# Performance work log

Hardware: AMD Instinct MI355X
Metric: run time of the kernel (lower is better)

The kernel has to match this reference:

```python
import jax, jax.numpy as jnp
import numpy as np

N = 768
C = 1024            # box_head representation size
HID = 256           # RePN hidden / gcn_hidden
HEADS1 = 4
K = 5               # topk neighbors
NEG_SLOPE = 0.2


def setup_inputs() -> dict:
    key = jax.random.key(0)
    ks = jax.random.split(key, 24)
    feats = jax.random.normal(ks[0], (N, C), dtype=jnp.float32)
    # valid boxes: x0<x1, y0<y1 inside an 800x800 image
    xy = jax.random.uniform(ks[1], (N, 2), dtype=jnp.float32) * 600.0
    wh = jax.random.uniform(ks[2], (N, 2), dtype=jnp.float32) * 150.0 + 2.0
    boxes = jnp.concatenate([xy, xy + wh], axis=1)
    s = 0.02
    # RePN fc1 weight [2C+4, HID] split into f1 / f2 / geom blocks (same math as concat)
    W1_f1 = jax.random.normal(ks[3], (C, HID), jnp.float32) * s
    W1_f2 = jax.random.normal(ks[4], (C, HID), jnp.float32) * s
    W1_g = jax.random.normal(ks[5], (4, HID), jnp.float32) * s
    b1 = jax.random.normal(ks[6], (HID,), jnp.float32) * s
    W2r = jax.random.normal(ks[7], (HID, 1), jnp.float32) * s
    b2r = jax.random.normal(ks[8], (1,), jnp.float32) * s
    # GAT1: (C+4) -> HID per head, 4 heads
    Wg1 = jax.random.normal(ks[9], (C + 4, HEADS1 * HID), jnp.float32) * s
    asrc1 = jax.random.normal(ks[10], (HEADS1, HID), jnp.float32) * s
    adst1 = jax.random.normal(ks[11], (HEADS1, HID), jnp.float32) * s
    bg1 = jax.random.normal(ks[12], (HEADS1 * HID,), jnp.float32) * s
    # GAT2: 4*HID -> 2, 1 head
    Wg2 = jax.random.normal(ks[13], (HEADS1 * HID, 2), jnp.float32) * s
    asrc2 = jax.random.normal(ks[14], (1, 2), jnp.float32) * s
    adst2 = jax.random.normal(ks[15], (1, 2), jnp.float32) * s
    bg2 = jax.random.normal(ks[16], (2,), jnp.float32) * s
    Wb1 = jax.random.normal(ks[17], (HEADS1 * HID + 4, HID // 2), jnp.float32) * s
    bb1 = jax.random.normal(ks[18], (HID // 2,), jnp.float32) * s
    Wb2 = jax.random.normal(ks[19], (HID // 2, 4), jnp.float32) * s
    bb2 = jax.random.normal(ks[20], (4,), jnp.float32) * s
    return {"feats": feats, "boxes": boxes, "img_h": 800, "img_w": 800,
            "W1_f1": W1_f1, "W1_f2": W1_f2, "W1_g": W1_g, "b1": b1,
            "W2r": W2r, "b2r": b2r,
            "Wg1": Wg1, "asrc1": asrc1, "adst1": adst1, "bg1": bg1,
            "Wg2": Wg2, "asrc2": asrc2, "adst2": adst2, "bg2": bg2,
            "Wb1": Wb1, "bb1": bb1, "Wb2": Wb2, "bb2": bb2}


def _box_geom(boxes, h, w):
    x0 = boxes[:, 0] / w
    y0 = boxes[:, 1] / h
    x1 = boxes[:, 2] / w
    y1 = boxes[:, 3] / h
    return jnp.stack([x0, y0, x1 - x0, y1 - y0], axis=1)


def _repn(feats, boxes, W1_f1, W1_f2, W1_g, b1, W2r, b2r):
    # fc1(cat([f1, f2, |b1-b2|])) decomposed as three matmuls (identical math).
    fa = feats @ W1_f1                          # [N, HID] contribution of row feature
    fb = feats @ W1_f2                          # [N, HID] contribution of col feature
    geom = jnp.abs(boxes[:, None, :] - boxes[None, :, :])  # [N, N, 4]
    h = jax.nn.relu(fa[:, None, :] + fb[None, :, :] + geom @ W1_g + b1)  # [N, N, HID]
    return (h @ W2r)[..., 0] + b2r[0]           # [N, N]


def _make_edges(rel):
    n = rel.shape[0]
    rn = rel - jnp.eye(n, dtype=rel.dtype) * 1e6
    _, idx = jax.lax.top_k(rn, K)               # [N, K] top-k neighbors per node
    dst = jnp.repeat(jnp.arange(n), K)
    src_row = dst                               # edge_index[0] in the torch code
    dst_row = idx.reshape(-1)                   # edge_index[1]
    # PyG GATConv default add_self_loops=True
    loops = jnp.arange(n)
    return jnp.concatenate([src_row, loops]), jnp.concatenate([dst_row, loops])


def _gat(x, e_src, e_dst, W, a_src, a_dst, bias, heads, out_c):
    n = x.shape[0]
    h = (x @ W).reshape(n, heads, out_c)        # [N, H, F]
    alpha_s = jnp.einsum('nhf,hf->nh', h, a_src)
    alpha_d = jnp.einsum('nhf,hf->nh', h, a_dst)
    e = alpha_s[e_src] + alpha_d[e_dst]         # [E, H]
    e = jax.nn.leaky_relu(e, NEG_SLOPE)
    m = jax.ops.segment_max(e, e_dst, num_segments=n)       # [N, H]
    ex = jnp.exp(e - m[e_dst])
    denom = jax.ops.segment_sum(ex, e_dst, num_segments=n)  # [N, H]
    attn = ex / denom[e_dst]
    msg = h[e_src] * attn[..., None]            # [E, H, F]
    out = jax.ops.segment_sum(msg, e_dst, num_segments=n)   # [N, H, F]
    return out.reshape(n, heads * out_c) + bias


def reference(feats, boxes, img_h, img_w,
              W1_f1, W1_f2, W1_g, b1, W2r, b2r,
              Wg1, asrc1, adst1, bg1, Wg2, asrc2, adst2, bg2,
              Wb1, bb1, Wb2, bb2):
    h_f = jnp.float32(img_h)
    w_f = jnp.float32(img_w)
    geom = _box_geom(boxes, h_f, w_f)                       # [N, 4]
    x = jnp.concatenate([feats, geom], axis=1)              # [N, C+4]
    rel = _repn(feats, boxes, W1_f1, W1_f2, W1_g, b1, W2r, b2r)
    e_src, e_dst = _make_edges(rel)
    h1 = jax.nn.relu(_gat(x, e_src, e_dst, Wg1, asrc1, adst1, bg1, HEADS1, HID))
    logits = _gat(h1, e_src, e_dst, Wg2, asrc2, adst2, bg2, 1, 2)  # [N, 2]
    prob_miss = jax.nn.softmax(logits, axis=1)[:, 1]
    reg_in = jnp.concatenate([h1, geom], axis=1)
    delta = jax.nn.relu(reg_in @ Wb1 + bb1) @ Wb2 + bb2     # [N, 4]
    px0, py0, px1, py1 = boxes[:, 0], boxes[:, 1], boxes[:, 2], boxes[:, 3]
    pw = px1 - px0
    ph = py1 - py0
    pcx = px0 + 0.5 * pw
    pcy = py0 + 0.5 * ph
    dx, dy, dw, dh = delta[:, 0], delta[:, 1], delta[:, 2], delta[:, 3]
    gcx = dx * pw + pcx
    gcy = dy * ph + pcy
    gw = jnp.exp(dw) * pw
    gh = jnp.exp(dh) * ph
    final_boxes = jnp.stack([gcx - 0.5 * gw, gcy - 0.5 * gh,
                             gcx + 0.5 * gw, gcy + 0.5 * gh], axis=1)
    # pack all outputs into one array: [N, N + 2 + 4 + 1]
    return jnp.concatenate([rel, logits, final_boxes, prob_miss[:, None]], axis=1)
```

## Files before the change

### kernel.cpp

```cpp
#include <hip/hip_runtime.h>
#include <hip/hip_fp16.h>
#include <float.h>

#define NN   768
#define CC   1024
#define HIDD 256
#define NH1  4
#define TOPK 5
#define NEDG (NN*TOPK + NN)
#define XW   (CC+4)
#define KP   1056
#define OUTW (NN+7)
#define G1W  (NH1*HIDD)
#define RH   128

typedef __attribute__((ext_vector_type(8))) short short8;
typedef __attribute__((ext_vector_type(4))) float f32x4;

__device__ unsigned short g_featsb[NN*CC];
__device__ unsigned short g_xb[NN*KP];
__device__ unsigned short g_wg1t[G1W*KP];
__device__ unsigned short g_w1f1t[HIDD*CC];
__device__ unsigned short g_w1f2t[HIDD*CC];
__device__ unsigned short g_wb1t[RH*KP];
__device__ unsigned short g_reginb[NN*KP];
__device__ __half g_fahp[2*NN*HIDD];
__device__ __half g_fbhp[2*NN*HIDD];
__device__ __half2 g_wrel[5*128];
__device__ __half g_relph[8*NN*NN];
__device__ float g_hgp[2*NN*G1W];
__device__ float g_hg[NN*G1W];
__device__ float g_as1[NN*NH1], g_ad1[NN*NH1];
__device__ int   g_idx[NN*TOPK];
__device__ int   g_off[NN+1], g_inlist[NEDG];
__device__ float g_h2[NN*2], g_as2[NN], g_ad2[NN];
__device__ float g_r1p[3*NN*RH];

__device__ __forceinline__ unsigned short f2bf(float f){
    unsigned int u = __float_as_uint(f);
    unsigned int r = (u + 0x7FFFu + ((u >> 16) & 1u)) >> 16;
    return (unsigned short)r;
}
__device__ __forceinline__ int edge_src(int eid){
    return (eid < NN*TOPK) ? (eid / TOPK) : (eid - NN*TOPK);
}
__device__ __forceinline__ __half2 h2max(__half2 a, __half2 b){
    __half2 r;
    asm("v_pk_max_f16 %0, %1, %2" : "=v"(r) : "v"(a), "v"(b));
    return r;
}

__device__ __forceinline__ void tconv(const float* __restrict__ W, int Kin, int N, int Kpad,
                                      unsigned short* __restrict__ O, int k0, int n0,
                                      int tx, int ty, float (*tile)[33]){
    #pragma unroll
    for (int i = 0; i < 4; i++){
        int k = k0 + ty + 8*i;
        tile[ty+8*i][tx] = (k < Kin) ? W[(size_t)k*N + n0 + tx] : 0.f;
    }
    __syncthreads();
    #pragma unroll
    for (int i = 0; i < 4; i++){
        int n = n0 + ty + 8*i;
        O[(size_t)n*Kpad + k0 + tx] = f2bf(tile[tx][ty+8*i]);
    }
}

__global__ void __launch_bounds__(256) k_prep_all(const float* __restrict__ feats,
                                                  const float* __restrict__ boxes,
                                                  const int* __restrict__ ih,
                                                  const int* __restrict__ iw,
                                                  const float* __restrict__ Wg1,
                                                  const float* __restrict__ W1f1,
                                                  const float* __restrict__ W1f2,
                                                  const float* __restrict__ Wb1,
                                                  const float* __restrict__ W1g,
                                                  const float* __restrict__ W2r){
    __shared__ float tile[32][33];
    int b = blockIdx.x, t = threadIdx.x;
    if (b < 384){
        int idx = b*256 + t;
        int n = idx >> 7, c8 = (idx & 127) << 3;
        const float* src = &feats[(size_t)n*CC + c8];
        float4 v0 = *(const float4*)src;
        float4 v1 = *(const float4*)(src + 4);
        uint4 pk;
        pk.x = (unsigned)f2bf(v0.x) | ((unsigned)f2bf(v0.y) << 16);
        pk.y = (unsigned)f2bf(v0.z) | ((unsigned)f2bf(v0.w) << 16);
        pk.z = (unsigned)f2bf(v1.x) | ((unsigned)f2bf(v1.y) << 16);
        pk.w = (unsigned)f2bf(v1.z) | ((unsigned)f2bf(v1.w) << 16);
        *(uint4*)&g_featsb[(size_t)n*CC + c8] = pk;
        *(uint4*)&g_xb[(size_t)n*KP + c8] = pk;
        return;
    }
    if (b < 387){
        int n = (b - 384)*256 + t;
        float w = (float)iw[0], h = (float)ih[0];
        float x0 = boxes[n*4+0]/w, y0 = boxes[n*4+1]/h;
        float x1 = boxes[n*4+2]/w, y1 = boxes[n*4+3]/h;
        float ge[4] = {x0, y0, x1-x0, y1-y0};
        #pragma unroll
        for (int c = 0; c < 4; c++){
            unsigned short bv = f2bf(ge[c]);
            g_xb[(size_t)n*KP + CC + c] = bv;
            g_reginb[(size_t)n*KP + CC + c] = bv;
        }
        for (int c = 4; c < KP - CC; c++){
            g_xb[(size_t)n*KP + CC + c] = 0;
            g_reginb[(size_t)n*KP + CC + c] = 0;
        }
        return;
    }
    if (b == 2087){
        for (int e = t; e < 5*128; e += 256){
            int r = e >> 7, fp = e & 127;
            const float* src = (r < 4) ? &W1g[r*HIDD + 2*fp] : &W2r[2*fp];
            g_wrel[e] = __floats2half2_rn(src[0], src[1]);
        }
        return;
    }
    int bb = b - 387;
    int tx = t & 31, ty = t >> 5;
    if (bb < 1056){
        int kt = bb % 33, nt = bb / 33;
        tconv(Wg1, XW, G1W, KP, g_wg1t, kt*32, nt*32, tx, ty, tile);
    } else if (bb < 1312){
        int b2 = bb - 1056;
        tconv(W1f1, CC, HIDD, CC, g_w1f1t, (b2%32)*32, (b2/32)*32, tx, ty, tile);
    } else if (bb < 1568){
        int b2 = bb - 1312;
        tconv(W1f2, CC, HIDD, CC, g_w1f2t, (b2%32)*32, (b2/32)*32, tx, ty, tile);
    } else {
        int b2 = bb - 1568;
        tconv(Wb1, XW, RH, KP, g_wb1t, (b2%33)*32, (b2/33)*32, tx, ty, tile);
    }
}

#define LSTR 40
__device__ __forceinline__ void mfma_gemm64(const unsigned short* __restrict__ A, int lda,
                                            const unsigned short* __restrict__ Bt, int ldb,
                                            int kstart, int Ks, float* __restrict__ Cf,
                                            __half* __restrict__ Ch, int ldc,
                                            const float* __restrict__ bias, bool relu,
                                            int bm, int bn,
                                            unsigned short* As, unsigned short* Bs){
    const int t = threadIdx.x;
    const int l = t & 63, w = t >> 6;
    const int wr = w >> 1, wc = w & 1;
    const int sr = t >> 2, sq = (t & 3) * 8;
    const size_t aoff = (size_t)(bm + sr)*lda + sq + (size_t)kstart*32;
    const size_t boff = (size_t)(bn + sr)*ldb + sq + (size_t)kstart*32;

    f32x4 acc[2][2];
    #pragma unroll
    for (int i = 0; i < 2; i++)
        #pragma unroll
        for (int j = 0; j < 2; j++)
            acc[i][j] = (f32x4){0.f,0.f,0.f,0.f};

    const int arow0 = (wr*32 + (l & 15)) * LSTR + ((l >> 4) * 8);
    const int brow0 = (wc*32 + (l & 15)) * LSTR + ((l >> 4) * 8);

    float4 a0v, b0v, a1v, b1v;
    a0v = *(const float4*)&A[aoff];            b0v = *(const float4*)&Bt[boff];
    a1v = *(const float4*)&A[aoff + 32];       b1v = *(const float4*)&Bt[boff + 32];

    for (int s = 0; s < Ks; s += 2){
        *(float4*)&As[sr*LSTR + sq] = a0v;
        *(float4*)&Bs[sr*LSTR + sq] = b0v;
        if (s + 2 < Ks){
            a0v = *(const float4*)&A[aoff + (size_t)(s+2)*32];
            b0v = *(const float4*)&Bt[boff + (size_t)(s+2)*32];
        }
        __syncthreads();
        {
            short8 fa0 = *(const short8*)&As[arow0];
            short8 fa1 = *(const short8*)&As[arow0 + 16*LSTR];
            short8 fb0 = *(const short8*)&Bs[brow0];
            short8 fb1 = *(const short8*)&Bs[brow0 + 16*LSTR];
            acc[0][0] = __builtin_amdgcn_mfma_f32_16x16x32_bf16(fa0, fb0, acc[0][0], 0, 0, 0);
            acc[0][1] = __builtin_amdgcn_mfma_f32_16x16x32_bf16(fa0, fb1, acc[0][1], 0, 0, 0);
            acc[1][0] = __builtin_amdgcn_mfma_f32_16x16x32_bf16(fa1, fb0, acc[1][0], 0, 0, 0);
            acc[1][1] = __builtin_amdgcn_mfma_f32_16x16x32_bf16(fa1, fb1, acc[1][1], 0, 0, 0);
        }
        __syncthreads();
        if (s + 1 >= Ks) break;
        *(float4*)&As[64*LSTR + sr*LSTR + sq] = a1v;
        *(float4*)&Bs[64*LSTR + sr*LSTR + sq] = b1v;
        if (s + 3 < Ks){
            a1v = *(const float4*)&A[aoff + (size_t)(s+3)*32];
            b1v = *(const float4*)&Bt[boff + (size_t)(s+3)*32];
        }
        __syncthreads();
        {
            short8 fa0 = *(const short8*)&As[64*LSTR + arow0];
            short8 fa1 = *(const short8*)&As[64*LSTR + arow0 + 16*LSTR];
            short8 fb0 = *(const short8*)&Bs[64*LSTR + brow0];
            short8 fb1 = *(const short8*)&Bs[64*LSTR + brow0 + 16*LSTR];
            acc[0][0] = __builtin_amdgcn_mfma_f32_16x16x32_bf16(fa0, fb0, acc[0][0], 0, 0, 0);
            acc[0][1] = __builtin_amdgcn_mfma_f32_16x16x32_bf16(fa0, fb1, acc[0][1], 0, 0, 0);
            acc[1][0] = __builtin_amdgcn_mfma_f32_16x16x32_bf16(fa1, fb0, acc[1][0], 0, 0, 0);
            acc[1][1] = __builtin_amdgcn_mfma_f32_16x16x32_bf16(fa1, fb1, acc[1][1], 0, 0, 0);
        }
        __syncthreads();
    }

    #pragma unroll
    for (int mi = 0; mi < 2; mi++){
        #pragma unroll
        for (int nj = 0; nj < 2; nj++){
            int col  = bn + wc*32 + nj*16 + (l & 15);
            int row0 = bm + wr*32 + mi*16 + ((l >> 4) * 4);
            float bv = bias ? bias[col] : 0.f;
            #pragma unroll
            for (int r = 0; r < 4; r++){
                float v = acc[mi][nj][r] + bv;
                if (relu) v = fmaxf(v, 0.f);
                if (Ch) Ch[(size_t)(row0+r)*ldc + col] = __float2half(v);
                else    Cf[(size_t)(row0+r)*ldc + col] = v;
            }
        }
    }
}

__global__ void __launch_bounds__(256) k_gemm_all(const float* __restrict__ b1){
    __shared__ unsigned short As[2*64*LSTR];
    __shared__ unsigned short Bs[2*64*LSTR];
    int b = blockIdx.x;
    if (b < 384){
        int p = b >> 7 >> 1;
        p = (b >= 192) ? 1 : 0;
        int bb = b - p*192;
        int ks = p ? 17 : 0, Ks = p ? 16 : 17;
        mfma_gemm64(g_xb, KP, g_wg1t, KP, ks, Ks,
                    g_hgp + (size_t)p*NN*G1W, nullptr, G1W, nullptr, false,
                    (bb>>4)*64, (bb&15)*64, As, Bs);
    } else if (b < 480){
        int q = b - 384;
        int p = (q >= 48) ? 1 : 0;
        int bb = q - p*48;
        mfma_gemm64(g_featsb, CC, g_w1f1t, CC, p*16, 16,
                    nullptr, g_fahp + (size_t)p*NN*HIDD, HIDD,
                    p ? nullptr : b1, false,
                    (bb>>2)*64, (bb&3)*64, As, Bs);
    } else {
        int q = b - 480;
        int p = (q >= 48) ? 1 : 0;
        int bb = q - p*48;
        mfma_gemm64(g_featsb, CC, g_w1f2t, CC, p*16, 16,
                    nullptr, g_fbhp + (size_t)p*NN*HIDD, HIDD, nullptr, false,
                    (bb>>2)*64, (bb&3)*64, As, Bs);
    }
}

__global__ void __launch_bounds__(256) k_gemm_r1(){
    __shared__ unsigned short As[2*64*LSTR];
    __shared__ unsigned short Bs[2*64*LSTR];
    int b = blockIdx.x;
    int slice = b / 24, bb = b % 24;
    mfma_gemm64(g_reginb, KP, g_wb1t, KP, slice*11, 11,
                g_r1p + (size_t)slice*NN*RH, nullptr, RH, nullptr, false,
                (bb>>1)*64, (bb&1)*64, As, Bs);
}

#define RSUB 32
__global__ void __launch_bounds__(256) __attribute__((amdgpu_waves_per_eu(4, 4)))
k_rel(const float* __restrict__ boxes){
    __shared__ __half2 sfa[16][68];
    __shared__ __half2 sfb[16][68];
    const int t = threadIdx.x;
    const int ib = blockIdx.y*64, jb = blockIdx.x*64;
    const int fc0 = blockIdx.z*RSUB;
    const int fpbase = blockIdx.z*16;
    const int rg = t >> 4, cg = t & 15;

    {
        const int fp = t & 15, nq = t >> 4;
        #pragma unroll
        for (int a2 = 0; a2 < 4; a2++){
            int node = nq*4 + a2;
            size_t o = (size_t)(ib+node)*HIDD + fc0 + 2*fp;
            size_t o2 = (size_t)(jb+node)*HIDD + fc0 + 2*fp;
            sfa[fp][node] = __hadd2(*(const __half2*)&g_fahp[o],
                                    *(const __half2*)&g_fahp[o + (size_t)NN*HIDD]);
            sfb[fp][node] = __hadd2(*(const __half2*)&g_fbhp[o2],
                                    *(const __half2*)&g_fbhp[o2 + (size_t)NN*HIDD]);
        }
    }

    float4 bi[4], bj[4];
    #pragma unroll
    for (int a = 0; a < 4; a++) bi[a] = *(const float4*)&boxes[(ib + rg*4 + a)*4];
    #pragma unroll
    for (int b = 0; b < 4; b++) bj[b] = *(const float4*)&boxes[(jb + cg*4 + b)*4];
    __half2 gg[4][4][4];
    #pragma unroll
    for (int a = 0; a < 4; a++)
        #pragma unroll
        for (int b = 0; b < 4; b++){
            const float* pa = (const float*)&bi[a];
            const float* pb = (const float*)&bj[b];
            #pragma unroll
            for (int c = 0; c < 4; c++){
                float gv = fabsf(pa[c] - pb[c]);
                gg[a][b][c] = __floats2half2_rn(gv, gv);
            }
        }
    __syncthreads();

    const __half2 hz = __floats2half2_rn(0.f, 0.f);
    __half2 acc2[4][4];
    #pragma unroll
    for (int a = 0; a < 4; a++)
        #pragma unroll
        for (int b = 0; b < 4; b++) acc2[a][b] = hz;

    #pragma unroll 4
    for (int fp = 0; fp < 16; fp++){
        __half2 w0  = g_wrel[0*128 + fpbase + fp];
        __half2 w1  = g_wrel[1*128 + fpbase + fp];
        __half2 w2  = g_wrel[2*128 + fpbase + fp];
        __half2 w3  = g_wrel[3*128 + fpbase + fp];
        __half2 wrv = g_wrel[4*128 + fpbase + fp];
        float4 fa_raw = *(const float4*)&sfa[fp][rg*4];
        float4 fb_raw = *(const float4*)&sfb[fp][cg*4];
        const __half2* FA = (const __half2*)&fa_raw;
        const __half2* FB = (const __half2*)&fb_raw;
        #pragma unroll
        for (int a = 0; a < 4; a++)
            #pragma unroll
            for (int b = 0; b < 4; b++){
                __half2 s = __hadd2(FA[a], FB[b]);
                s = __hfma2(gg[a][b][0], w0, s);
                s = __hfma2(gg[a][b][1], w1, s);
                s = __hfma2(gg[a][b][2], w2, s);
                s = __hfma2(gg[a][b][3], w3, s);
                s = h2max(s, hz);
                acc2[a][b] = __hfma2(s, wrv, acc2[a][b]);
            }
    }

    __half* po = g_relph + (size_t)blockIdx.z*NN*NN + (size_t)ib*NN + jb;
    #pragma unroll
    for (int a = 0; a < 4; a++){
        unsigned short u[4];
        #pragma unroll
        for (int b = 0; b < 4; b++){
            float sum = __low2float(acc2[a][b]) + __high2float(acc2[a][b]);
            u[b] = __half_as_ushort(__float2half(sum));
        }
        uint2 o;
        o.x = (unsigned)u[0] | ((unsigned)u[1] << 16);
        o.y = (unsigned)u[2] | ((unsigned)u[3] << 16);
        *(uint2*)&po[(size_t)(rg*4+a)*NN + cg*4] = o;
    }
}

__global__ void __launch_bounds__(64) k_topk(const float* __restrict__ asrc,
                                             const float* __restrict__ adst,
                                             const float* __restrict__ b2r,
                                             float* __restrict__ out){
    int i = blockIdx.x, t = threadIdx.x;
    float* row = out + (size_t)i*OUTW;

    float ss[4] = {0,0,0,0}, sd[4] = {0,0,0,0};
    const float* hp0 = g_hgp + (size_t)i*G1W;
    const float* hp1 = hp0 + (size_t)NN*G1W;
    float* hout = g_hg + (size_t)i*G1W;
    #pragma unroll
    for (int k = 0; k < 16; k++){
        const int h = k >> 2;
        int u = t + 64*k;
        float hv = hp0[u] + hp1[u];
        hout[u] = hv;
        ss[h] += hv * asrc[u];
        sd[h] += hv * adst[u];
    }
    #pragma unroll
    for (int h = 0; h < 4; h++)
        for (int off = 32; off; off >>= 1){
            ss[h] += __shfl_down(ss[h], off);
            sd[h] += __shfl_down(sd[h], off);
        }
    if (t == 0){
        #pragma unroll
        for (int h = 0; h < 4; h++){ g_as1[i*4+h] = ss[h]; g_ad1[i*4+h] = sd[h]; }
    }

    const __half* p0 = g_relph + (size_t)i*NN;
    float bb = b2r[0];
    float rv[12];
    #pragma unroll
    for (int kk = 0; kk < 6; kk++){
        int j2 = 128*kk + 2*t;
        float sx = bb, sy = bb;
        #pragma unroll
        for (int z = 0; z < 8; z++){
            __half2 hv = *(const __half2*)&p0[(size_t)z*NN*NN + j2];
            sx += __low2float(hv);
            sy += __high2float(hv);
        }
        rv[2*kk]   = sx;
        rv[2*kk+1] = sy;
        row[j2]   = sx;
        row[j2+1] = sy;
    }

    int sel[TOPK];
    for (int k = 0; k < TOPK; k++){
        float bv = -FLT_MAX; int bj = NN;
        #pragma unroll
        for (int kk = 0; kk < 12; kk++){
            int j = 128*(kk >> 1) + 2*t + (kk & 1);
            if (j == i) continue;
            bool used = false;
            #pragma unroll
            for (int u = 0; u < TOPK; u++) if (u < k && sel[u] == j) used = true;
            if (used) continue;
            float v = rv[kk];
            if (v > bv || (v == bv && j < bj)){ bv = v; bj = j; }
        }
        for (int off = 32; off; off >>= 1){
            float v2 = __shfl_down(bv, off);
            int   j2 = __shfl_down(bj, off);
            if (v2 > bv || (v2 == bv && j2 < bj)){ bv = v2; bj = j2; }
        }
        bv = __shfl(bv, 0); bj = __shfl(bj, 0);
        sel[k] = bj;
    }
    if (t < TOPK) g_idx[i*TOPK + t] = sel[t];
}

__global__ void __launch_bounds__(1024) k_csr(){
    __shared__ int sa[NN], sb[NN];
    int t = threadIdx.x;
    for (int i = t; i < NN; i += 1024) sa[i] = 0;
    __syncthreads();
    for (int e = t; e < NEDG; e += 1024){
        int d = (e < NN*TOPK) ? g_idx[e] : (e - NN*TOPK);
        atomicAdd(&sa[d], 1);
    }
    __syncthreads();
    int* src = sa; int* dst = sb;
    for (int off = 1; off < NN; off <<= 1){
        for (int i = t; i < NN; i += 1024)
            dst[i] = src[i] + ((i >= off) ? src[i-off] : 0);
        __syncthreads();
        int* tmp = src; src = dst; dst = tmp;
    }
    for (int i = t; i < NN; i += 1024) g_off[i] = (i ? src[i-1] : 0);
    if (t == 0) g_off[NN] = src[NN-1];
    for (int i = t; i < NN; i += 1024) dst[i] = 0;
    __syncthreads();
    for (int e = t; e < NEDG; e += 1024){
        int d = (e < NN*TOPK) ? g_idx[e] : (e - NN*TOPK);
        int pos = atomicAdd(&dst[d], 1);
        int base = d ? src[d-1] : 0;
        g_inlist[base + pos] = e;
    }
}

__global__ void __launch_bounds__(256) k_gat1(const float* __restrict__ bg1,
                                              const float* __restrict__ Wg2,
                                              const float* __restrict__ as2w,
                                              const float* __restrict__ ad2w){
    __shared__ float sattn[NN*4];
    __shared__ float sden[4];
    __shared__ float sp0[4], sp1[4];
    int n = blockIdx.x, t = threadIdx.x;
    int beg = g_off[n], deg = g_off[n+1] - beg;
    int w = t >> 6, l = t & 63;

    {
        float adn = g_ad1[n*NH1 + w];
        float s = 0.f;
        for (int e = l; e < deg; e += 64){
            int src = edge_src(g_inlist[beg + e]);
            float ev = g_as1[src*NH1 + w] + adn;
            ev = (ev > 0.f) ? ev : 0.2f*ev;
            float ex = expf(ev);
            sattn[e*4 + w] = ex;
            s += ex;
        }
        for (int off = 32; off; off >>= 1) s += __shfl_down(s, off);
        if (l == 0) sden[w] = s;
    }
    __syncthreads();

    float rd[NH1];
    #pragma unroll
    for (int h = 0; h < NH1; h++) rd[h] = 1.f / sden[h];
    float acc[NH1] = {0.f,0.f,0.f,0.f};
    for (int e = 0; e < deg; e++){
        int src = edge_src(g_inlist[beg + e]);
        const float* hr = g_hg + (size_t)src*G1W;
        #pragma unroll
        for (int h = 0; h < NH1; h++)
            acc[h] += sattn[e*4 + h] * hr[h*HIDD + t];
    }
    float p0 = 0.f, p1 = 0.f;
    #pragma unroll
    for (int h = 0; h < NH1; h++){
        int c = h*HIDD + t;
        float v = acc[h]*rd[h] + bg1[c];
        v = fmaxf(v, 0.f);
        g_reginb[(size_t)n*KP + c] = f2bf(v);
        p0 += v * Wg2[c*2 + 0];
        p1 += v * Wg2[c*2 + 1];
    }
    for (int off = 32; off; off >>= 1){
        p0 += __shfl_down(p0, off);
        p1 += __shfl_down(p1, off);
    }
    if (l == 0){ sp0[w] = p0; sp1[w] = p1; }
    __syncthreads();
    if (t == 0){
        float h0 = sp0[0]+sp0[1]+sp0[2]+sp0[3];
        float h1 = sp1[0]+sp1[1]+sp1[2]+sp1[3];
        g_h2[n*2+0] = h0; g_h2[n*2+1] = h1;
        g_as2[n] = h0*as2w[0] + h1*as2w[1];
        g_ad2[n] = h0*ad2w[0] + h1*ad2w[1];
    }
}

__global__ void __launch_bounds__(64) k_tail(const float* __restrict__ bg2,
                                             const float* __restrict__ Wb2,
                                             const float* __restrict__ bb1,
                                             const float* __restrict__ bb2,
                                             const float* __restrict__ boxes,
                                             float* __restrict__ out){
    int n = blockIdx.x, t = threadIdx.x;

    int beg = g_off[n], deg = g_off[n+1] - beg;
    float adn = g_ad2[n];
    float den = 0.f, l0 = 0.f, l1 = 0.f;
    for (int e = t; e < deg; e += 64){
        int src = edge_src(g_inlist[beg + e]);
        float ev = g_as2[src] + adn;
        ev = (ev > 0.f) ? ev : 0.2f*ev;
        float ex = expf(ev);
        den += ex;
        l0 += ex * g_h2[src*2+0];
        l1 += ex * g_h2[src*2+1];
    }
    #pragma unroll
    for (int off = 32; off; off >>= 1){
        den += __shfl_xor(den, off);
        l0  += __shfl_xor(l0, off);
        l1  += __shfl_xor(l1, off);
    }

    float d0 = 0.f, d1 = 0.f, d2 = 0.f, d3 = 0.f;
    const float* q0 = g_r1p + (size_t)n*RH;
    #pragma unroll
    for (int kk = 0; kk < 2; kk++){
        int k = t + 64*kk;
        float r = q0[k] + q0[k + (size_t)NN*RH] + q0[k + 2*(size_t)NN*RH] + bb1[k];
        r = fmaxf(r, 0.f);
        float4 wv = *(const float4*)&Wb2[k*4];
        d0 += r*wv.x; d1 += r*wv.y; d2 += r*wv.z; d3 += r*wv.w;
    }
    #pragma unroll
    for (int off = 32; off; off >>= 1){
        d0 += __shfl_xor(d0, off);
        d1 += __shfl_xor(d1, off);
        d2 += __shfl_xor(d2, off);
        d3 += __shfl_xor(d3, off);
    }

    if (t == 0){
        float rdv = 1.f / den;
        float L0 = l0*rdv + bg2[0];
        float L1 = l1*rdv + bg2[1];
        out[(size_t)n*OUTW + NN + 0] = L0;
        out[(size_t)n*OUTW + NN + 1] = L1;
        float m = fmaxf(L0, L1);
        float e0 = expf(L0 - m), e1 = expf(L1 - m);
        out[(size_t)n*OUTW + NN + 6] = e1 / (e0 + e1);

        float dd0 = d0 + bb2[0], dd1 = d1 + bb2[1];
        float dd2 = d2 + bb2[2], dd3 = d3 + bb2[3];
        float px0 = boxes[n*4+0], py0 = boxes[n*4+1];
        float px1 = boxes[n*4+2], py1 = boxes[n*4+3];
        float pw = px1 - px0, ph = py1 - py0;
        float pcx = px0 + 0.5f*pw, pcy = py0 + 0.5f*ph;
        float gcx = dd0*pw + pcx, gcy = dd1*ph + pcy;
        float gw = expf(dd2)*pw,  gh = expf(dd3)*ph;
        out[(size_t)n*OUTW + NN + 2] = gcx - 0.5f*gw;
        out[(size_t)n*OUTW + NN + 3] = gcy - 0.5f*gh;
        out[(size_t)n*OUTW + NN + 4] = gcx + 0.5f*gw;
        out[(size_t)n*OUTW + NN + 5] = gcy + 0.5f*gh;
    }
}

extern "C" void kernel_launch(void* const* d_in, const int* in_sizes, int n_in,
                              void* d_out, int out_size, void* d_ws, size_t ws_size,
                              hipStream_t stream){
    const float* feats = (const float*)d_in[0];
    const float* boxes = (const float*)d_in[1];
    const int*   ih    = (const int*)  d_in[2];
    const int*   iw    = (const int*)  d_in[3];
    const float* W1f1  = (const float*)d_in[4];
    const float* W1f2  = (const float*)d_in[5];
    const float* W1g   = (const float*)d_in[6];
    const float* b1    = (const float*)d_in[7];
    const float* W2r   = (const float*)d_in[8];
    const float* b2r   = (const float*)d_in[9];
    const float* Wg1   = (const float*)d_in[10];
    const float* asrc1 = (const float*)d_in[11];
    const float* adst1 = (const float*)d_in[12];
    const float* bg1   = (const float*)d_in[13];
    const float* Wg2   = (const float*)d_in[14];
    const float* asrc2 = (const float*)d_in[15];
    const float* adst2 = (const float*)d_in[16];
    const float* bg2   = (const float*)d_in[17];
    const float* Wb1   = (const float*)d_in[18];
    const float* bb1   = (const float*)d_in[19];
    const float* Wb2   = (const float*)d_in[20];
    const float* bb2   = (const float*)d_in[21];
    float* out = (float*)d_out;

    k_prep_all<<<2088, 256, 0, stream>>>(feats, boxes, ih, iw, Wg1, W1f1, W1f2, Wb1, W1g, W2r);
    k_gemm_all<<<576, 256, 0, stream>>>(b1);
    k_rel<<<dim3(NN/64, NN/64, 8), 256, 0, stream>>>(boxes);
    k_topk<<<NN, 64, 0, stream>>>(asrc1, adst1, b2r, out);
    k_csr<<<1, 1024, 0, stream>>>();
    k_gat1<<<NN, 256, 0, stream>>>(bg1, Wg2, asrc2, adst2);
    k_gemm_r1<<<72, 256, 0, stream>>>();
    k_tail<<<NN, 64, 0, stream>>>(bg2, Wb2, bb1, bb2, boxes, out);
}
```

Measured before the change: 94.48 us.

## Drop CSR build and bbox-regressor GEMM, scan topk per node and fuse regressor

Removes the single-block CSR kernel. Each GAT block now finds its incoming edges by scanning every node's top-k list in shared memory. The bf16 transpose of Wb1 and the separate MFMA GEMM for the regressor's first layer are also removed; k_tail computes that 1028x128 layer per node by reading fp32 Wb1 directly. This cuts two launches and the serial CSR kernel, at the cost of an O(N) scan per block that is done twice and a scalar per-node GEMV that rereads Wb1 768 times.

```diff
diff --git a/kernel.cpp b/kernel.cpp
--- a/kernel.cpp
+++ b/kernel.cpp
@@ -7,7 +7,6 @@
 #define HIDD 256
 #define NH1  4
 #define TOPK 5
-#define NEDG (NN*TOPK + NN)
 #define XW   (CC+4)
 #define KP   1056
 #define OUTW (NN+7)
@@ -22,8 +21,7 @@
 __device__ unsigned short g_wg1t[G1W*KP];
 __device__ unsigned short g_w1f1t[HIDD*CC];
 __device__ unsigned short g_w1f2t[HIDD*CC];
-__device__ unsigned short g_wb1t[RH*KP];
-__device__ unsigned short g_reginb[NN*KP];
+__device__ unsigned short g_reginb[NN*XW];
 __device__ __half g_fahp[2*NN*HIDD];
 __device__ __half g_fbhp[2*NN*HIDD];
 __device__ __half2 g_wrel[5*128];
@@ -32,17 +30,12 @@
 __device__ float g_hg[NN*G1W];
 __device__ float g_as1[NN*NH1], g_ad1[NN*NH1];
 __device__ int   g_idx[NN*TOPK];
-__device__ int   g_off[NN+1], g_inlist[NEDG];
 __device__ float g_h2[NN*2], g_as2[NN], g_ad2[NN];
-__device__ float g_r1p[3*NN*RH];
 
 __device__ __forceinline__ unsigned short f2bf(float f){
     unsigned int u = __float_as_uint(f);
     unsigned int r = (u + 0x7FFFu + ((u >> 16) & 1u)) >> 16;
     return (unsigned short)r;
-}
-__device__ __forceinline__ int edge_src(int eid){
-    return (eid < NN*TOPK) ? (eid / TOPK) : (eid - NN*TOPK);
 }
 __device__ __forceinline__ __half2 h2max(__half2 a, __half2 b){
     __half2 r;
@@ -73,7 +66,6 @@
                                                   const float* __restrict__ Wg1,
                                                   const float* __restrict__ W1f1,
                                                   const float* __restrict__ W1f2,
-                                                  const float* __restrict__ Wb1,
                                                   const float* __restrict__ W1g,
                                                   const float* __restrict__ W2r){
     __shared__ float tile[32][33];
@@ -100,18 +92,13 @@
         float x1 = boxes[n*4+2]/w, y1 = boxes[n*4+3]/h;
         float ge[4] = {x0, y0, x1-x0, y1-y0};
         #pragma unroll
-        for (int c = 0; c < 4; c++){
-            unsigned short bv = f2bf(ge[c]);
-            g_xb[(size_t)n*KP + CC + c] = bv;
-            g_reginb[(size_t)n*KP + CC + c] = bv;
-        }
-        for (int c = 4; c < KP - CC; c++){
+        for (int c = 0; c < 4; c++)
+            g_xb[(size_t)n*KP + CC + c] = f2bf(ge[c]);
+        for (int c = 4; c < KP - CC; c++)
             g_xb[(size_t)n*KP + CC + c] = 0;
-            g_reginb[(size_t)n*KP + CC + c] = 0;
-        }
         return;
     }
-    if (b == 2087){
+    if (b == 387){
         for (int e = t; e < 5*128; e += 256){
             int r = e >> 7, fp = e & 127;
             const float* src = (r < 4) ? &W1g[r*HIDD + 2*fp] : &W2r[2*fp];
@@ -119,7 +106,7 @@
         }
         return;
     }
-    int bb = b - 387;
+    int bb = b - 388;
     int tx = t & 31, ty = t >> 5;
     if (bb < 1056){
         int kt = bb % 33, nt = bb / 33;
@@ -127,12 +114,9 @@
     } else if (bb < 1312){
         int b2 = bb - 1056;
         tconv(W1f1, CC, HIDD, CC, g_w1f1t, (b2%32)*32, (b2/32)*32, tx, ty, tile);
-    } else if (bb < 1568){
+    } else {
         int b2 = bb - 1312;
         tconv(W1f2, CC, HIDD, CC, g_w1f2t, (b2%32)*32, (b2/32)*32, tx, ty, tile);
-    } else {
-        int b2 = bb - 1568;
-        tconv(Wb1, XW, RH, KP, g_wb1t, (b2%33)*32, (b2/33)*32, tx, ty, tile);
     }
 }
 
@@ -228,8 +212,7 @@
     __shared__ unsigned short Bs[2*64*LSTR];
     int b = blockIdx.x;
     if (b < 384){
-        int p = b >> 7 >> 1;
-        p = (b >= 192) ? 1 : 0;
+        int p = (b >= 192) ? 1 : 0;
         int bb = b - p*192;
         int ks = p ? 17 : 0, Ks = p ? 16 : 17;
         mfma_gemm64(g_xb, KP, g_wg1t, KP, ks, Ks,
@@ -253,16 +236,6 @@
     }
 }
 
-__global__ void __launch_bounds__(256) k_gemm_r1(){
-    __shared__ unsigned short As[2*64*LSTR];
-    __shared__ unsigned short Bs[2*64*LSTR];
-    int b = blockIdx.x;
-    int slice = b / 24, bb = b % 24;
-    mfma_gemm64(g_reginb, KP, g_wb1t, KP, slice*11, 11,
-                g_r1p + (size_t)slice*NN*RH, nullptr, RH, nullptr, false,
-                (bb>>1)*64, (bb&1)*64, As, Bs);
-}
-
 #define RSUB 32
 __global__ void __launch_bounds__(256) __attribute__((amdgpu_waves_per_eu(4, 4)))
 k_rel(const float* __restrict__ boxes){
@@ -431,51 +404,37 @@
     if (t < TOPK) g_idx[i*TOPK + t] = sel[t];
 }
 
-__global__ void __launch_bounds__(1024) k_csr(){
-    __shared__ int sa[NN], sb[NN];
-    int t = threadIdx.x;
-    for (int i = t; i < NN; i += 1024) sa[i] = 0;
-    __syncthreads();
-    for (int e = t; e < NEDG; e += 1024){
-        int d = (e < NN*TOPK) ? g_idx[e] : (e - NN*TOPK);
-        atomicAdd(&sa[d], 1);
-    }
-    __syncthreads();
-    int* src = sa; int* dst = sb;
-    for (int off = 1; off < NN; off <<= 1){
-        for (int i = t; i < NN; i += 1024)
-            dst[i] = src[i] + ((i >= off) ? src[i-off] : 0);
-        __syncthreads();
-        int* tmp = src; src = dst; dst = tmp;
-    }
-    for (int i = t; i < NN; i += 1024) g_off[i] = (i ? src[i-1] : 0);
-    if (t == 0) g_off[NN] = src[NN-1];
-    for (int i = t; i < NN; i += 1024) dst[i] = 0;
-    __syncthreads();
-    for (int e = t; e < NEDG; e += 1024){
-        int d = (e < NN*TOPK) ? g_idx[e] : (e - NN*TOPK);
-        int pos = atomicAdd(&dst[d], 1);
-        int base = d ? src[d-1] : 0;
-        g_inlist[base + pos] = e;
-    }
-}
-
 __global__ void __launch_bounds__(256) k_gat1(const float* __restrict__ bg1,
                                               const float* __restrict__ Wg2,
                                               const float* __restrict__ as2w,
-                                              const float* __restrict__ ad2w){
+                                              const float* __restrict__ ad2w,
+                                              const float* __restrict__ boxes,
+                                              const int* __restrict__ ih,
+                                              const int* __restrict__ iw){
     __shared__ float sattn[NN*4];
+    __shared__ int   sedge[NN];
+    __shared__ int   scnt;
     __shared__ float sden[4];
     __shared__ float sp0[4], sp1[4];
     int n = blockIdx.x, t = threadIdx.x;
-    int beg = g_off[n], deg = g_off[n+1] - beg;
     int w = t >> 6, l = t & 63;
+
+    if (t == 0){ scnt = 1; sedge[0] = n; }
+    __syncthreads();
+    for (int s = t; s < NN; s += 256){
+        if (s == n) continue;
+        const int* ip = &g_idx[s*TOPK];
+        bool hit = (ip[0]==n) | (ip[1]==n) | (ip[2]==n) | (ip[3]==n) | (ip[4]==n);
+        if (hit){ int p = atomicAdd(&scnt, 1); sedge[p] = s; }
+    }
+    __syncthreads();
+    int deg = scnt;
 
     {
         float adn = g_ad1[n*NH1 + w];
         float s = 0.f;
         for (int e = l; e < deg; e += 64){
-            int src = edge_src(g_inlist[beg + e]);
+            int src = sedge[e];
             float ev = g_as1[src*NH1 + w] + adn;
             ev = (ev > 0.f) ? ev : 0.2f*ev;
             float ex = expf(ev);
@@ -492,7 +451,7 @@
     for (int h = 0; h < NH1; h++) rd[h] = 1.f / sden[h];
     float acc[NH1] = {0.f,0.f,0.f,0.f};
     for (int e = 0; e < deg; e++){
-        int src = edge_src(g_inlist[beg + e]);
+        int src = sedge[e];
         const float* hr = g_hg + (size_t)src*G1W;
         #pragma unroll
         for (int h = 0; h < NH1; h++)
@@ -504,7 +463,7 @@
         int c = h*HIDD + t;
         float v = acc[h]*rd[h] + bg1[c];
         v = fmaxf(v, 0.f);
-        g_reginb[(size_t)n*KP + c] = f2bf(v);
+        g_reginb[(size_t)n*XW + c] = f2bf(v);
         p0 += v * Wg2[c*2 + 0];
         p1 += v * Wg2[c*2 + 1];
     }
@@ -521,21 +480,41 @@
         g_as2[n] = h0*as2w[0] + h1*as2w[1];
         g_ad2[n] = h0*ad2w[0] + h1*ad2w[1];
     }
+    if (t < 4){
+        float w2 = (float)iw[0], h2v = (float)ih[0];
+        float x0 = boxes[n*4+0]/w2, y0 = boxes[n*4+1]/h2v;
+        float x1 = boxes[n*4+2]/w2, y1 = boxes[n*4+3]/h2v;
+        float ge[4] = {x0, y0, x1-x0, y1-y0};
+        g_reginb[(size_t)n*XW + CC + t] = f2bf(ge[t]);
+    }
 }
 
 __global__ void __launch_bounds__(64) k_tail(const float* __restrict__ bg2,
+                                             const float* __restrict__ Wb1,
+                                             const float* __restrict__ bb1,
                                              const float* __restrict__ Wb2,
-                                             const float* __restrict__ bb1,
                                              const float* __restrict__ bb2,
                                              const float* __restrict__ boxes,
                                              float* __restrict__ out){
+    __shared__ int sedge[NN];
+    __shared__ int scnt;
     int n = blockIdx.x, t = threadIdx.x;
 
-    int beg = g_off[n], deg = g_off[n+1] - beg;
+    if (t == 0){ scnt = 1; sedge[0] = n; }
+    __syncthreads();
+    for (int s = t; s < NN; s += 64){
+        if (s == n) continue;
+        const int* ip = &g_idx[s*TOPK];
+        bool hit = (ip[0]==n) | (ip[1]==n) | (ip[2]==n) | (ip[3]==n) | (ip[4]==n);
+        if (hit){ int p = atomicAdd(&scnt, 1); sedge[p] = s; }
+    }
+    __syncthreads();
+    int deg = scnt;
+
     float adn = g_ad2[n];
     float den = 0.f, l0 = 0.f, l1 = 0.f;
     for (int e = t; e < deg; e += 64){
-        int src = edge_src(g_inlist[beg + e]);
+        int src = sedge[e];
         float ev = g_as2[src] + adn;
         ev = (ev > 0.f) ? ev : 0.2f*ev;
         float ex = expf(ev);
@@ -550,16 +529,24 @@
         l1  += __shfl_xor(l1, off);
     }
 
-    float d0 = 0.f, d1 = 0.f, d2 = 0.f, d3 = 0.f;
-    const float* q0 = g_r1p + (size_t)n*RH;
-    #pragma unroll
-    for (int kk = 0; kk < 2; kk++){
-        int k = t + 64*kk;
-        float r = q0[k] + q0[k + (size_t)NN*RH] + q0[k + 2*(size_t)NN*RH] + bb1[k];
-        r = fmaxf(r, 0.f);
-        float4 wv = *(const float4*)&Wb2[k*4];
-        d0 += r*wv.x; d1 += r*wv.y; d2 += r*wv.z; d3 += r*wv.w;
-    }
+    float s0 = 0.f, s1 = 0.f;
+    const unsigned int* rp = (const unsigned int*)&g_reginb[(size_t)n*XW];
+    for (int cu = 0; cu < XW/2; cu++){
+        unsigned int pk = rp[cu];
+        float rA = __uint_as_float(pk << 16);
+        float rB = __uint_as_float(pk & 0xffff0000u);
+        int c = cu*2;
+        s0 += rA * Wb1[(size_t)c*RH + t]      + rB * Wb1[(size_t)(c+1)*RH + t];
+        s1 += rA * Wb1[(size_t)c*RH + t + 64] + rB * Wb1[(size_t)(c+1)*RH + t + 64];
+    }
+    float r0 = fmaxf(s0 + bb1[t], 0.f);
+    float r1v = fmaxf(s1 + bb1[t+64], 0.f);
+    float4 w0v = *(const float4*)&Wb2[t*4];
+    float4 w1v = *(const float4*)&Wb2[(t+64)*4];
+    float d0 = r0*w0v.x + r1v*w1v.x;
+    float d1 = r0*w0v.y + r1v*w1v.y;
+    float d2 = r0*w0v.z + r1v*w1v.z;
+    float d3 = r0*w0v.w + r1v*w1v.w;
     #pragma unroll
     for (int off = 32; off; off >>= 1){
         d0 += __shfl_xor(d0, off);
@@ -620,12 +607,10 @@
     const float* bb2   = (const float*)d_in[21];
     float* out = (float*)d_out;
 
-    k_prep_all<<<2088, 256, 0, stream>>>(feats, boxes, ih, iw, Wg1, W1f1, W1f2, Wb1, W1g, W2r);
+    k_prep_all<<<1956, 256, 0, stream>>>(feats, boxes, ih, iw, Wg1, W1f1, W1f2, W1g, W2r);
     k_gemm_all<<<576, 256, 0, stream>>>(b1);
     k_rel<<<dim3(NN/64, NN/64, 8), 256, 0, stream>>>(boxes);
     k_topk<<<NN, 64, 0, stream>>>(asrc1, adst1, b2r, out);
-    k_csr<<<1, 1024, 0, stream>>>();
-    k_gat1<<<NN, 256, 0, stream>>>(bg1, Wg2, asrc2, adst2);
-    k_gemm_r1<<<72, 256, 0, stream>>>();
-    k_tail<<<NN, 64, 0, stream>>>(bg2, Wb2, bb1, bb2, boxes, out);
-}
+    k_gat1<<<NN, 256, 0, stream>>>(bg1, Wg2, asrc2, adst2, boxes, ih, iw);
+    k_tail<<<NN, 64, 0, stream>>>(bg2, Wb1, bb1, Wb2, bb2, boxes, out);
+}
```

After: 150.5 us. 59.3% more time.
